# Kernel optimization log

Hardware: AMD Instinct MI355X
Metric: run time of the kernel (lower is better)

Reference implementation:

```python
import jax, jax.numpy as jnp
import numpy as np

V = 50000; C0 = 2000; C1 = 10000   # vocab and adaptive-softmax cutoffs
E = 512; H = 1024; B = 32; T = 128
H1 = H // 4; H2 = H // 16           # div_val = 4.0 per source formula
S1 = C1 - C0; S2 = V - C1


def setup_inputs() -> dict:
    key = jax.random.key(0)
    ks = jax.random.split(key, 12)
    # lengths sorted descending, max length == T (required by output.view(b*(T-1),-1))
    lengths = jnp.sort(jax.random.randint(ks[0], (B,), T // 2, T + 1))[::-1]
    lengths = lengths.at[0].set(T).astype(jnp.int64)
    x = jax.random.randint(ks[1], (B, T), 1, V)
    x = jnp.where(jnp.arange(T)[None, :] < lengths[:, None], x, 0).astype(jnp.int64)  # PAD=0 beyond length
    emb = (jax.random.normal(ks[2], (V, E), jnp.float32) * 0.02).at[0].set(0.0)  # padding_idx=0
    w_ih = jax.random.normal(ks[3], (3 * H, E), jnp.float32) * 0.02
    w_hh = jax.random.normal(ks[4], (3 * H, H), jnp.float32) * 0.02
    b_ih = jnp.zeros((3 * H,), jnp.float32)
    b_hh = jnp.zeros((3 * H,), jnp.float32)
    head_w = jax.random.normal(ks[5], (C0 + 2, H), jnp.float32) * 0.02   # shortlist + 2 cluster logits
    p1 = jax.random.normal(ks[6], (H1, H), jnp.float32) * 0.02
    t1 = jax.random.normal(ks[7], (S1, H1), jnp.float32) * 0.02
    p2 = jax.random.normal(ks[8], (H2, H), jnp.float32) * 0.02
    t2 = jax.random.normal(ks[9], (S2, H2), jnp.float32) * 0.02
    hidden = jnp.zeros((1, B, H), jnp.float32)
    return dict(x=x, lengths=lengths, hidden=hidden, emb=emb, w_ih=w_ih, w_hh=w_hh,
                b_ih=b_ih, b_hh=b_hh, head_w=head_w, p1=p1, t1=t1, p2=p2, t2=t2)


def gru_masked(inp, h0, w_ih, w_hh, b_ih, b_hh, lengths):
    """Torch GRU on packed sequence of lengths-1: frozen hidden + zero outputs past length."""
    xp = jnp.einsum('bte,ge->btg', inp, w_ih) + b_ih  # [B, T-1, 3H] input projections

    def step(h, args):
        xpt, t = args
        hp = h @ w_hh.T + b_hh
        xr, xz, xn = jnp.split(xpt, 3, axis=-1)
        hr, hz, hn = jnp.split(hp, 3, axis=-1)
        r = jax.nn.sigmoid(xr + hr)
        z = jax.nn.sigmoid(xz + hz)
        n = jnp.tanh(xn + r * hn)
        h_new = (1.0 - z) * n + z * h
        valid = (t < lengths - 1)[:, None]
        h = jnp.where(valid, h_new, h)          # freeze hidden past sequence end
        y = jnp.where(valid, h, 0.0)            # pad_packed_sequence zero-fills
        return h, y

    steps = jnp.arange(inp.shape[1])
    hT, ys = jax.lax.scan(step, h0, (jnp.swapaxes(xp, 0, 1), steps))
    return jnp.swapaxes(ys, 0, 1), hT  # [B, T-1, H], [B, H]


def adaptive_loss(out, targets, head_w, p1, t1, p2, t2):
    """AdaptiveLogSoftmaxWithLoss: mean NLL over shortlist + 2 tail clusters."""
    N = out.shape[0]
    head_lp = jax.nn.log_softmax(out @ head_w.T, axis=-1)  # [N, C0+2]
    idx = jnp.arange(N)
    lp_short = head_lp[idx, jnp.clip(targets, 0, C0 - 1)]

    def cluster_lp(p, t, ci, lo, size):
        tail_lp = jax.nn.log_softmax((out @ p.T) @ t.T, axis=-1)  # [N, size]
        rel = jnp.clip(targets - lo, 0, size - 1)
        return head_lp[:, C0 + ci] + tail_lp[idx, rel]

    lp1 = cluster_lp(p1, t1, 0, C0, S1)
    lp2 = cluster_lp(p2, t2, 1, C1, S2)
    logp = jnp.where(targets < C0, lp_short, jnp.where(targets < C1, lp1, lp2))
    return -jnp.mean(logp)


def reference(x, lengths, hidden, emb, w_ih, w_hh, b_ih, b_hh, head_w, p1, t1, p2, t2):
    inp = emb[x][:, :T - 1]  # dropout=0.0 -> identity
    ys, hT = gru_masked(inp, hidden[0], w_ih, w_hh, b_ih, b_hh, lengths)
    out = ys.reshape(B * (T - 1), H)
    targets = x[:, 1:].reshape(-1)
    loss = adaptive_loss(out, targets, head_w, p1, t1, p2, t2)
    return loss, hT[None]
```

## Files before the change

kernel.cpp:

```cpp
#include <hip/hip_runtime.h>
#include <math.h>

#define VV   50000
#define CC0  2000
#define CC1  10000
#define ED   512
#define HD   1024
#define BBATCH 32
#define TT   128
#define HH1  256
#define HH2  64
#define SS1  8000
#define SS2  40000
#define NR   4064
#define G3   3072

#define OFF_XP   0ull
#define OFF_YSB  12484608ull
#define OFF_HB   14565376ull
#define OFF_HT   14598144ull
#define OFF_P1B  14630912ull
#define OFF_P2B  15151104ull
#define OFF_WHB  15281152ull
#define OFF_T1B  16306176ull
#define OFF_PP1  17330176ull
#define OFF_PP2  17461248ull
#define OFF_SUM  17494016ull
#define OFF_LOSS (OFF_SUM + 6ull*4064ull)
#define OFF_INT  (OFF_LOSS + 64ull)

#define ZERO_N (6*4064 + 64)
#define NBG 64

typedef __attribute__((ext_vector_type(8))) __bf16 bf16x8;
typedef __attribute__((ext_vector_type(4))) float f32x4;
typedef __attribute__((ext_vector_type(4))) unsigned int u32x4;
typedef unsigned long long u64;
typedef unsigned short u16;
struct ull2s { u64 x, y; };

__device__ __forceinline__ u16 f2bf(float f) {
    unsigned u = __builtin_bit_cast(unsigned, f);
    u += 0x7fff + ((u >> 16) & 1);
    return (u16)(u >> 16);
}

__global__ void init_k(const float* __restrict__ hidden, u16* __restrict__ hb0,
                       float* __restrict__ zreg, int* __restrict__ cnt1,
                       int* __restrict__ cnt2, int* __restrict__ bar)
{
    int i = blockIdx.x * 256 + threadIdx.x;
    if (i < BBATCH * HD) hb0[i] = f2bf(hidden[i]);
    int zi = i - BBATCH * HD;
    if (zi >= 0 && zi < ZERO_N) zreg[zi] = 0.f;
    if (zi == ZERO_N) { *cnt1 = 0; *cnt2 = 0; }
    int bi = zi - (ZERO_N + 1);
    if (bi >= 0 && bi < 2048) bar[bi] = 0;
}

__global__ void prep_k(const int* __restrict__ x, int* __restrict__ targets,
                       int* __restrict__ hselc, int* __restrict__ list1,
                       int* __restrict__ list2, int* __restrict__ cnt1, int* __restrict__ cnt2)
{
    int n = blockIdx.x * 256 + threadIdx.x;
    if (n >= NR) return;
    int b = n / 127, t = n % 127;
    int tgt = x[b * TT + t + 1];
    targets[n] = tgt;
    hselc[n] = (tgt < CC0) ? tgt : ((tgt < CC1) ? CC0 : CC0 + 1);
    if (tgt >= CC0 && tgt < CC1) list1[atomicAdd(cnt1, 1)] = n;
    else if (tgt >= CC1)         list2[atomicAdd(cnt2, 1)] = n;
}

__global__ void cvt_bf16_k(const float* __restrict__ src, u16* __restrict__ dst, int n4)
{
    int i = blockIdx.x * 256 + threadIdx.x;
    if (i >= n4) return;
    float4 f = *(const float4*)(src + 4 * (size_t)i);
    union { u16 h[4]; u64 v; } u;
    u.h[0] = f2bf(f.x); u.h[1] = f2bf(f.y); u.h[2] = f2bf(f.z); u.h[3] = f2bf(f.w);
    *(u64*)&dst[4 * (size_t)i] = u.v;
}

__global__ void __launch_bounds__(256)
gemm_xp_k(const int* __restrict__ x, const float* __restrict__ emb,
          const float* __restrict__ w_ih, const float* __restrict__ b_ih,
          float* __restrict__ xp)
{
    __shared__ float smem[2 * 16 * 132];
    __shared__ int tok[128];
    float* As = smem;
    float* Ws = smem + 16 * 132;
    const int tid = threadIdx.x;
    const int rbase = blockIdx.x * 128;
    const int cbase = blockIdx.y * 128;
    const int rg = tid >> 4, cg = tid & 15;
    const int rl = tid >> 1;
    const int kk0 = (tid & 1) * 8;

    if (tid < 128) {
        int r = rbase + tid;
        tok[tid] = (r < NR) ? x[(r & 31) * TT + (r >> 5)] : -1;
    }
    __syncthreads();

    float acc[8][8];
#pragma unroll
    for (int i = 0; i < 8; i++)
#pragma unroll
        for (int j = 0; j < 8; j++) acc[i][j] = 0.f;

    for (int k0 = 0; k0 < ED; k0 += 16) {
        int tk = tok[rl];
        float4 a0 = make_float4(0,0,0,0), a1 = a0;
        if (tk >= 0) {
            const float* ap = emb + (size_t)tk * ED + k0 + kk0;
            a0 = *(const float4*)(ap);
            a1 = *(const float4*)(ap + 4);
        }
        As[(kk0+0)*132 + rl] = a0.x; As[(kk0+1)*132 + rl] = a0.y;
        As[(kk0+2)*132 + rl] = a0.z; As[(kk0+3)*132 + rl] = a0.w;
        As[(kk0+4)*132 + rl] = a1.x; As[(kk0+5)*132 + rl] = a1.y;
        As[(kk0+6)*132 + rl] = a1.z; As[(kk0+7)*132 + rl] = a1.w;

        const float* wp = w_ih + (size_t)(cbase + rl) * ED + k0 + kk0;
        float4 w0 = *(const float4*)(wp);
        float4 w1 = *(const float4*)(wp + 4);
        Ws[(kk0+0)*132 + rl] = w0.x; Ws[(kk0+1)*132 + rl] = w0.y;
        Ws[(kk0+2)*132 + rl] = w0.z; Ws[(kk0+3)*132 + rl] = w0.w;
        Ws[(kk0+4)*132 + rl] = w1.x; Ws[(kk0+5)*132 + rl] = w1.y;
        Ws[(kk0+6)*132 + rl] = w1.z; Ws[(kk0+7)*132 + rl] = w1.w;
        __syncthreads();
#pragma unroll
        for (int kk = 0; kk < 16; kk++) {
            float4 va0 = *(float4*)&As[kk*132 + rg*8];
            float4 va1 = *(float4*)&As[kk*132 + rg*8 + 4];
            float4 vw0 = *(float4*)&Ws[kk*132 + cg*8];
            float4 vw1 = *(float4*)&Ws[kk*132 + cg*8 + 4];
            float av[8] = {va0.x,va0.y,va0.z,va0.w,va1.x,va1.y,va1.z,va1.w};
            float wv[8] = {vw0.x,vw0.y,vw0.z,vw0.w,vw1.x,vw1.y,vw1.z,vw1.w};
#pragma unroll
            for (int i = 0; i < 8; i++)
#pragma unroll
                for (int j = 0; j < 8; j++) acc[i][j] += av[i] * wv[j];
        }
        __syncthreads();
    }
#pragma unroll
    for (int i = 0; i < 8; i++) {
        int r = rbase + rg*8 + i;
        if (r >= NR) continue;
#pragma unroll
        for (int j = 0; j < 8; j++) {
            int c = cbase + cg*8 + j;
            xp[(size_t)r * G3 + c] = acc[i][j] + b_ih[c];
        }
    }
}

template<int EPI, int BFP32>
__global__ void __launch_bounds__(256)
mfma_gemm_k(const u16* __restrict__ Ab, const void* __restrict__ Bsrc,
            int Mdirect, int N, int K,
            const int* __restrict__ rowmap, const int* __restrict__ cntp,
            u16* __restrict__ outB, int ldo,
            float* __restrict__ gsum, float* __restrict__ gsel,
            const int* __restrict__ selcol, const int* __restrict__ targets, int lo)
{
    const int M = cntp ? *cntp : Mdirect;
    const int rbase = blockIdx.x * 128;
    if (rbase >= M) return;
    const int cbase = blockIdx.y * 128;

    __shared__ u16 As[128 * 40];
    __shared__ u16 Bs[128 * 40];
    __shared__ const u16* aptr[128];
    __shared__ int rown[128];
    __shared__ float redl[128 * 2];

    const int tid = threadIdx.x;
    if (tid < 128) {
        int rid = -1;
        if (rbase + tid < M) rid = rowmap ? rowmap[rbase + tid] : (rbase + tid);
        rown[tid] = rid;
        aptr[tid] = (rid >= 0) ? (Ab + (size_t)rid * K) : nullptr;
    }
    __syncthreads();

    const int lane = tid & 63, wid = tid >> 6;
    const int n16 = lane & 15, quad = lane >> 4;
    const int m0 = (wid >> 1) * 64, n0 = (wid & 1) * 64;
    const int i = tid >> 1, half = tid & 1;

    f32x4 acc[4][4];
#pragma unroll
    for (int a = 0; a < 4; a++)
#pragma unroll
        for (int b = 0; b < 4; b++) acc[a][b] = (f32x4){0.f, 0.f, 0.f, 0.f};

    for (int k0 = 0; k0 < K; k0 += 32) {
        const u16* ap = aptr[i];
        u32x4 a0 = {0,0,0,0}, a1 = a0;
        if (ap) {
            a0 = *(const u32x4*)(ap + k0 + half * 16);
            a1 = *(const u32x4*)(ap + k0 + half * 16 + 8);
        }
        u32x4 b0 = {0,0,0,0}, b1 = b0;
        int c = cbase + i;
        if (c < N) {
            if (BFP32) {
                const float* bp = (const float*)Bsrc + (size_t)c * K + k0 + half * 16;
                float4 f0 = *(const float4*)(bp);
                float4 f1 = *(const float4*)(bp + 4);
                float4 f2 = *(const float4*)(bp + 8);
                float4 f3 = *(const float4*)(bp + 12);
                union { u16 h[16]; u32x4 v[2]; } u;
                u.h[0]=f2bf(f0.x); u.h[1]=f2bf(f0.y); u.h[2]=f2bf(f0.z); u.h[3]=f2bf(f0.w);
                u.h[4]=f2bf(f1.x); u.h[5]=f2bf(f1.y); u.h[6]=f2bf(f1.z); u.h[7]=f2bf(f1.w);
                u.h[8]=f2bf(f2.x); u.h[9]=f2bf(f2.y); u.h[10]=f2bf(f2.z); u.h[11]=f2bf(f2.w);
                u.h[12]=f2bf(f3.x); u.h[13]=f2bf(f3.y); u.h[14]=f2bf(f3.z); u.h[15]=f2bf(f3.w);
                b0 = u.v[0]; b1 = u.v[1];
            } else {
                const u16* bp = (const u16*)Bsrc + (size_t)c * K + k0 + half * 16;
                b0 = *(const u32x4*)(bp);
                b1 = *(const u32x4*)(bp + 8);
            }
        }
        __syncthreads();
        *(u32x4*)&As[i * 40 + half * 16]     = a0;
        *(u32x4*)&As[i * 40 + half * 16 + 8] = a1;
        *(u32x4*)&Bs[i * 40 + half * 16]     = b0;
        *(u32x4*)&Bs[i * 40 + half * 16 + 8] = b1;
        __syncthreads();

        bf16x8 av[4], bv[4];
#pragma unroll
        for (int mi = 0; mi < 4; mi++)
            av[mi] = *(const bf16x8*)&As[(m0 + mi * 16 + n16) * 40 + quad * 8];
#pragma unroll
        for (int ni = 0; ni < 4; ni++)
            bv[ni] = *(const bf16x8*)&Bs[(n0 + ni * 16 + n16) * 40 + quad * 8];
#pragma unroll
        for (int mi = 0; mi < 4; mi++)
#pragma unroll
            for (int ni = 0; ni < 4; ni++)
                acc[mi][ni] = __builtin_amdgcn_mfma_f32_16x16x32_bf16(
                    av[mi], bv[ni], acc[mi][ni], 0, 0, 0);
    }

    __syncthreads();
    if (EPI == 0) {
#pragma unroll
        for (int mi = 0; mi < 4; mi++)
#pragma unroll
            for (int ni = 0; ni < 4; ni++)
#pragma unroll
                for (int r = 0; r < 4; r++) {
                    int row = rbase + m0 + mi * 16 + quad * 4 + r;
                    int col = cbase + n0 + ni * 16 + n16;
                    if (row < M && col < N)
                        outB[(size_t)row * ldo + col] = f2bf(acc[mi][ni][r]);
                }
    } else {
#pragma unroll
        for (int mi = 0; mi < 4; mi++)
#pragma unroll
            for (int r = 0; r < 4; r++) {
                int lrow = m0 + mi * 16 + quad * 4 + r;
                int nid = rown[lrow];
                float s = 0.f;
                if (nid >= 0) {
                    int sc = (EPI == 1) ? selcol[nid] : (targets[nid] - lo);
#pragma unroll
                    for (int ni = 0; ni < 4; ni++) {
                        int col = cbase + n0 + ni * 16 + n16;
                        if (col < N) {
                            float v = acc[mi][ni][r];
                            s += __expf(v);
                            if (col == sc) gsel[nid] = v;
                        }
                    }
                }
                s += __shfl_xor(s, 1);
                s += __shfl_xor(s, 2);
                s += __shfl_xor(s, 4);
                s += __shfl_xor(s, 8);
                if (n16 == 0) redl[lrow * 2 + (wid & 1)] = s;
            }
        __syncthreads();
        if (tid < 128) {
            int nid = rown[tid];
            if (nid >= 0) atomicAdd(&gsum[nid], redl[tid * 2] + redl[tid * 2 + 1]);
        }
    }
}

__global__ void __launch_bounds__(128, 1)
gru_persist_k(const float* __restrict__ xp, const float* __restrict__ hidden,
              u16* __restrict__ hb0, u16* __restrict__ hb1,
              const float* __restrict__ w_hh, const float* __restrict__ b_hh,
              const int* __restrict__ lengths, u16* __restrict__ ys,
              float* __restrict__ hT, int* __restrict__ arr)
{
    __shared__ u16 Blds[48 * 1032];
    const int tid = threadIdx.x;
    const int bid = blockIdx.x;
    const int j0 = bid * 16;
    const int lane = tid & 63, wid = tid >> 6;
    const int n16 = lane & 15, quad = lane >> 4;

    for (int idx = tid; idx < 48 * 1024; idx += 128) {
        int r = idx >> 10, k = idx & 1023;
        int g = r >> 4, c = r & 15;
        Blds[r * 1032 + k] = f2bf(w_hh[(size_t)(g * HD + j0 + c) * HD + k]);
    }

    const int col = j0 + n16;
    float bh0 = b_hh[col], bh1 = b_hh[HD + col], bh2 = b_hh[2 * HD + col];
    float hold[4];
    int len[4];
#pragma unroll
    for (int r = 0; r < 4; r++) {
        int b = wid * 16 + quad * 4 + r;
        len[r] = lengths[b];
        hold[r] = hidden[b * HD + col];
    }
    __syncthreads();

    for (int t = 0; t < TT - 1; t++) {
        const u16* hb = (t & 1) ? hb1 : hb0;
        u16* hbn = (t & 1) ? hb0 : hb1;

        float xrv[4], xzv[4], xnv[4];
#pragma unroll
        for (int r = 0; r < 4; r++) {
            int b = wid * 16 + quad * 4 + r;
            const float* xpt = xp + ((size_t)t * BBATCH + b) * G3 + col;
            xrv[r] = xpt[0]; xzv[r] = xpt[HD]; xnv[r] = xpt[2 * HD];
        }

        const u16* arow = hb + (size_t)(wid * 16 + n16) * HD + quad * 8;
        u64 apf[64];
#pragma unroll
        for (int ks = 0; ks < 32; ks++) {
            apf[2*ks]   = __hip_atomic_load((const u64*)(arow + ks*32),
                                            __ATOMIC_RELAXED, __HIP_MEMORY_SCOPE_AGENT);
            apf[2*ks+1] = __hip_atomic_load((const u64*)(arow + ks*32 + 4),
                                            __ATOMIC_RELAXED, __HIP_MEMORY_SCOPE_AGENT);
        }

        f32x4 acc0 = {0.f, 0.f, 0.f, 0.f}, acc1 = acc0, acc2 = acc0;
        const int boff = n16 * 1032 + quad * 8;
#pragma unroll
        for (int ks = 0; ks < 32; ks++) {
            ull2s av2; av2.x = apf[2*ks]; av2.y = apf[2*ks+1];
            bf16x8 av = __builtin_bit_cast(bf16x8, av2);
            bf16x8 b0 = *(const bf16x8*)&Blds[boff + ks*32];
            bf16x8 b1 = *(const bf16x8*)&Blds[16*1032 + boff + ks*32];
            bf16x8 b2 = *(const bf16x8*)&Blds[32*1032 + boff + ks*32];
            acc0 = __builtin_amdgcn_mfma_f32_16x16x32_bf16(av, b0, acc0, 0, 0, 0);
            acc1 = __builtin_amdgcn_mfma_f32_16x16x32_bf16(av, b1, acc1, 0, 0, 0);
            acc2 = __builtin_amdgcn_mfma_f32_16x16x32_bf16(av, b2, acc2, 0, 0, 0);
        }

#pragma unroll
        for (int r = 0; r < 4; r++) {
            int b = wid * 16 + quad * 4 + r;
            float hr = acc0[r] + bh0, hz = acc1[r] + bh1, hn = acc2[r] + bh2;
            float rg = 1.f / (1.f + __expf(-(xrv[r] + hr)));
            float zg = 1.f / (1.f + __expf(-(xzv[r] + hz)));
            float nv = tanhf(xnv[r] + rg * hn);
            bool valid = t < (len[r] - 1);
            float hnew = valid ? (1.f - zg) * nv + zg * hold[r] : hold[r];
            hold[r] = hnew;
            __hip_atomic_store(hbn + (size_t)b * HD + col, f2bf(hnew),
                               __ATOMIC_RELAXED, __HIP_MEMORY_SCOPE_AGENT);
            ys[((size_t)b * 127 + t) * HD + col] = f2bf(valid ? hnew : 0.f);
            if (t == TT - 2) hT[b * HD + col] = hnew;
        }

        __syncthreads();
        if (tid < 64) {
            if (tid == 0) {
                __builtin_amdgcn_s_waitcnt(0);
                __hip_atomic_store(&arr[bid * 32], t + 1, __ATOMIC_RELAXED,
                                   __HIP_MEMORY_SCOPE_AGENT);
            }
            int guard = 0;
            while (__hip_atomic_load(&arr[tid * 32], __ATOMIC_RELAXED,
                                     __HIP_MEMORY_SCOPE_AGENT) < t + 1
                   && guard < (1 << 20)) {
                __builtin_amdgcn_s_sleep(1);
                guard++;
            }
        }
        asm volatile("" ::: "memory");
        __syncthreads();
    }
}

__global__ void finish_k(const float* __restrict__ hsum, const float* __restrict__ hsel,
                         const float* __restrict__ t1sum, const float* __restrict__ t1sel,
                         const float* __restrict__ t2sum, const float* __restrict__ t2sel,
                         const int* __restrict__ targets, float* __restrict__ losssum)
{
    __shared__ float red[256];
    int n = blockIdx.x * 256 + threadIdx.x;
    float lp = 0.f;
    if (n < NR) {
        lp = hsel[n] - logf(hsum[n]);
        int tgt = targets[n];
        if (tgt >= CC1)      lp += t2sel[n] - logf(t2sum[n]);
        else if (tgt >= CC0) lp += t1sel[n] - logf(t1sum[n]);
    }
    red[threadIdx.x] = lp;
    __syncthreads();
    for (int s = 128; s > 0; s >>= 1) {
        if (threadIdx.x < s) red[threadIdx.x] += red[threadIdx.x + s];
        __syncthreads();
    }
    if (threadIdx.x == 0) atomicAdd(losssum, red[0]);
}

__global__ void out_k(const float* __restrict__ losssum, const float* __restrict__ hT,
                      float* __restrict__ out)
{
    int i = blockIdx.x * 256 + threadIdx.x;
    if (i == 0) out[0] = -losssum[0] / (float)NR;
    if (i < BBATCH * HD) out[1 + i] = hT[i];
}

extern "C" void kernel_launch(void* const* d_in, const int* in_sizes, int n_in,
                              void* d_out, int out_size, void* d_ws, size_t ws_size,
                              hipStream_t stream)
{
    const int*   x       = (const int*)d_in[0];
    const int*   lengths = (const int*)d_in[1];
    const float* hidden  = (const float*)d_in[2];
    const float* emb     = (const float*)d_in[3];
    const float* w_ih    = (const float*)d_in[4];
    const float* w_hh    = (const float*)d_in[5];
    const float* b_ih    = (const float*)d_in[6];
    const float* b_hh    = (const float*)d_in[7];
    const float* head_w  = (const float*)d_in[8];
    const float* p1      = (const float*)d_in[9];
    const float* t1      = (const float*)d_in[10];
    const float* p2      = (const float*)d_in[11];
    const float* t2      = (const float*)d_in[12];

    float* ws = (float*)d_ws;
    float* xp    = ws + OFF_XP;
    u16*   ysb   = (u16*)(ws + OFF_YSB);
    u16*   hb0   = (u16*)(ws + OFF_HB);
    u16*   hb1   = hb0 + BBATCH * HD;
    float* hT    = ws + OFF_HT;
    u16*   p1b   = (u16*)(ws + OFF_P1B);
    u16*   p2b   = (u16*)(ws + OFF_P2B);
    u16*   whb   = (u16*)(ws + OFF_WHB);
    u16*   t1b   = (u16*)(ws + OFF_T1B);
    u16*   pp1b  = (u16*)(ws + OFF_PP1);
    u16*   pp2b  = (u16*)(ws + OFF_PP2);
    float* hsum  = ws + OFF_SUM;
    float* hsel  = hsum + 4064;
    float* t1sum = hsel + 4064;
    float* t1sel = t1sum + 4064;
    float* t2sum = t1sel + 4064;
    float* t2sel = t2sum + 4064;
    float* losss = ws + OFF_LOSS;
    int* ib      = (int*)(ws + OFF_INT);
    int* targets = ib;
    int* hselc   = ib + 4064;
    int* list1   = ib + 2 * 4064;
    int* list2   = ib + 3 * 4064;
    int* cnt1    = ib + 4 * 4064;
    int* cnt2    = cnt1 + 1;
    int* bar     = ib + 5 * 4064;

    float* out = (float*)d_out;

    init_k<<<232, 256, 0, stream>>>(hidden, hb0, hsum, cnt1, cnt2, bar);
    prep_k<<<16, 256, 0, stream>>>(x, targets, hselc, list1, list2, cnt1, cnt2);

    cvt_bf16_k<<<(512512 + 255) / 256, 256, 0, stream>>>(head_w, whb, 512512);
    cvt_bf16_k<<<(512000 + 255) / 256, 256, 0, stream>>>(t1, t1b, 512000);
    cvt_bf16_k<<<(65536 + 255) / 256, 256, 0, stream>>>(p1, pp1b, 65536);
    cvt_bf16_k<<<(16384 + 255) / 256, 256, 0, stream>>>(p2, pp2b, 16384);

    gemm_xp_k<<<dim3(32, 24), 256, 0, stream>>>(x, emb, w_ih, b_ih, xp);

    gru_persist_k<<<NBG, 128, 0, stream>>>(xp, hidden, hb0, hb1, w_hh, b_hh,
                                           lengths, ysb, hT, bar);

    mfma_gemm_k<0, 0><<<dim3(32, 2), 256, 0, stream>>>(
        ysb, pp1b, NR, HH1, HD, nullptr, nullptr, p1b, HH1,
        nullptr, nullptr, nullptr, nullptr, 0);
    mfma_gemm_k<0, 0><<<dim3(32, 1), 256, 0, stream>>>(
        ysb, pp2b, NR, HH2, HD, nullptr, nullptr, p2b, HH2,
        nullptr, nullptr, nullptr, nullptr, 0);
    mfma_gemm_k<1, 0><<<dim3(32, 16), 256, 0, stream>>>(
        ysb, whb, NR, CC0 + 2, HD, nullptr, nullptr, nullptr, 0,
        hsum, hsel, hselc, nullptr, 0);
    mfma_gemm_k<2, 0><<<dim3(32, 63), 256, 0, stream>>>(
        p1b, t1b, 0, SS1, HH1, list1, cnt1, nullptr, 0,
        t1sum, t1sel, nullptr, targets, CC0);
    mfma_gemm_k<2, 1><<<dim3(32, 313), 256, 0, stream>>>(
        p2b, t2, 0, SS2, HH2, list2, cnt2, nullptr, 0,
        t2sum, t2sel, nullptr, targets, CC1);

    finish_k<<<16, 256, 0, stream>>>(hsum, hsel, t1sum, t1sel, t2sum, t2sel,
                                     targets, losss);
    out_k<<<128, 256, 0, stream>>>(losss, hT, out);
}
```

Baseline: 1.540 ms.

## Move input projection GEMM to bf16 MFMA and pre-convert t2 to bf16

Replaces the fp32 FMA embedding×w_ih GEMM with a bf16 gather kernel, a w_ih conversion, and the existing MFMA GEMM using a new epilogue that adds the bias and writes fp32 xp. It also converts t2 to bf16 once into the xp buffer after the GRU has consumed it, so the tail-2 GEMM uses the bf16 B path. The aim is to cut the cost of the pre-GRU projection with matrix cores, in exchange for bf16 rounding of the GRU inputs and several workspace buffers being reused (embA in the ysb slot, w_ih in the head_w slot before head_w is converted).

New measurement: 1.427 ms. -7.4%, faster.

```diff
diff --git a/kernel.cpp b/kernel.cpp
--- a/kernel.cpp
+++ b/kernel.cpp
@@ -82,80 +82,22 @@
     *(u64*)&dst[4 * (size_t)i] = u.v;
 }
 
-__global__ void __launch_bounds__(256)
-gemm_xp_k(const int* __restrict__ x, const float* __restrict__ emb,
-          const float* __restrict__ w_ih, const float* __restrict__ b_ih,
-          float* __restrict__ xp)
-{
-    __shared__ float smem[2 * 16 * 132];
-    __shared__ int tok[128];
-    float* As = smem;
-    float* Ws = smem + 16 * 132;
-    const int tid = threadIdx.x;
-    const int rbase = blockIdx.x * 128;
-    const int cbase = blockIdx.y * 128;
-    const int rg = tid >> 4, cg = tid & 15;
-    const int rl = tid >> 1;
-    const int kk0 = (tid & 1) * 8;
-
-    if (tid < 128) {
-        int r = rbase + tid;
-        tok[tid] = (r < NR) ? x[(r & 31) * TT + (r >> 5)] : -1;
-    }
-    __syncthreads();
-
-    float acc[8][8];
-#pragma unroll
-    for (int i = 0; i < 8; i++)
-#pragma unroll
-        for (int j = 0; j < 8; j++) acc[i][j] = 0.f;
-
-    for (int k0 = 0; k0 < ED; k0 += 16) {
-        int tk = tok[rl];
-        float4 a0 = make_float4(0,0,0,0), a1 = a0;
-        if (tk >= 0) {
-            const float* ap = emb + (size_t)tk * ED + k0 + kk0;
-            a0 = *(const float4*)(ap);
-            a1 = *(const float4*)(ap + 4);
-        }
-        As[(kk0+0)*132 + rl] = a0.x; As[(kk0+1)*132 + rl] = a0.y;
-        As[(kk0+2)*132 + rl] = a0.z; As[(kk0+3)*132 + rl] = a0.w;
-        As[(kk0+4)*132 + rl] = a1.x; As[(kk0+5)*132 + rl] = a1.y;
-        As[(kk0+6)*132 + rl] = a1.z; As[(kk0+7)*132 + rl] = a1.w;
-
-        const float* wp = w_ih + (size_t)(cbase + rl) * ED + k0 + kk0;
-        float4 w0 = *(const float4*)(wp);
-        float4 w1 = *(const float4*)(wp + 4);
-        Ws[(kk0+0)*132 + rl] = w0.x; Ws[(kk0+1)*132 + rl] = w0.y;
-        Ws[(kk0+2)*132 + rl] = w0.z; Ws[(kk0+3)*132 + rl] = w0.w;
-        Ws[(kk0+4)*132 + rl] = w1.x; Ws[(kk0+5)*132 + rl] = w1.y;
-        Ws[(kk0+6)*132 + rl] = w1.z; Ws[(kk0+7)*132 + rl] = w1.w;
-        __syncthreads();
-#pragma unroll
-        for (int kk = 0; kk < 16; kk++) {
-            float4 va0 = *(float4*)&As[kk*132 + rg*8];
-            float4 va1 = *(float4*)&As[kk*132 + rg*8 + 4];
-            float4 vw0 = *(float4*)&Ws[kk*132 + cg*8];
-            float4 vw1 = *(float4*)&Ws[kk*132 + cg*8 + 4];
-            float av[8] = {va0.x,va0.y,va0.z,va0.w,va1.x,va1.y,va1.z,va1.w};
-            float wv[8] = {vw0.x,vw0.y,vw0.z,vw0.w,vw1.x,vw1.y,vw1.z,vw1.w};
-#pragma unroll
-            for (int i = 0; i < 8; i++)
-#pragma unroll
-                for (int j = 0; j < 8; j++) acc[i][j] += av[i] * wv[j];
-        }
-        __syncthreads();
-    }
-#pragma unroll
-    for (int i = 0; i < 8; i++) {
-        int r = rbase + rg*8 + i;
-        if (r >= NR) continue;
-#pragma unroll
-        for (int j = 0; j < 8; j++) {
-            int c = cbase + cg*8 + j;
-            xp[(size_t)r * G3 + c] = acc[i][j] + b_ih[c];
-        }
-    }
+__global__ void emb_gather_k(const int* __restrict__ x, const float* __restrict__ emb,
+                             u16* __restrict__ embA)
+{
+    int idx = blockIdx.x * 256 + threadIdx.x;
+    if (idx >= NR * 64) return;
+    int n = idx >> 6;
+    int kk = (idx & 63) << 3;
+    int b = n & 31, t = n >> 5;
+    int tok = x[b * TT + t];
+    const float* ap = emb + (size_t)tok * ED + kk;
+    float4 f0 = *(const float4*)ap;
+    float4 f1 = *(const float4*)(ap + 4);
+    union { u16 h[8]; u32x4 v; } u;
+    u.h[0] = f2bf(f0.x); u.h[1] = f2bf(f0.y); u.h[2] = f2bf(f0.z); u.h[3] = f2bf(f0.w);
+    u.h[4] = f2bf(f1.x); u.h[5] = f2bf(f1.y); u.h[6] = f2bf(f1.z); u.h[7] = f2bf(f1.w);
+    *(u32x4*)&embA[(size_t)n * ED + kk] = u.v;
 }
 
 template<int EPI, int BFP32>
@@ -260,6 +202,18 @@
                     int col = cbase + n0 + ni * 16 + n16;
                     if (row < M && col < N)
                         outB[(size_t)row * ldo + col] = f2bf(acc[mi][ni][r]);
+                }
+    } else if (EPI == 3) {
+#pragma unroll
+        for (int mi = 0; mi < 4; mi++)
+#pragma unroll
+            for (int ni = 0; ni < 4; ni++)
+#pragma unroll
+                for (int r = 0; r < 4; r++) {
+                    int row = rbase + m0 + mi * 16 + quad * 4 + r;
+                    int col = cbase + n0 + ni * 16 + n16;
+                    if (row < M && col < N)
+                        gsum[(size_t)row * ldo + col] = acc[mi][ni][r] + gsel[col];
                 }
     } else {
 #pragma unroll
@@ -476,20 +430,30 @@
     int* cnt2    = cnt1 + 1;
     int* bar     = ib + 5 * 4064;
 
+    u16* embA = (u16*)(ws + OFF_YSB);
+    u16* wihb = (u16*)(ws + OFF_WHB);
+    u16* t2b  = (u16*)(ws + OFF_XP);
+
     float* out = (float*)d_out;
 
     init_k<<<232, 256, 0, stream>>>(hidden, hb0, hsum, cnt1, cnt2, bar);
     prep_k<<<16, 256, 0, stream>>>(x, targets, hselc, list1, list2, cnt1, cnt2);
+
+    emb_gather_k<<<(NR * 64 + 255) / 256, 256, 0, stream>>>(x, emb, embA);
+    cvt_bf16_k<<<(393216 + 255) / 256, 256, 0, stream>>>(w_ih, wihb, 393216);
+    mfma_gemm_k<3, 0><<<dim3(32, 24), 256, 0, stream>>>(
+        embA, wihb, NR, G3, ED, nullptr, nullptr, nullptr, G3,
+        xp, (float*)b_ih, nullptr, nullptr, 0);
 
     cvt_bf16_k<<<(512512 + 255) / 256, 256, 0, stream>>>(head_w, whb, 512512);
     cvt_bf16_k<<<(512000 + 255) / 256, 256, 0, stream>>>(t1, t1b, 512000);
     cvt_bf16_k<<<(65536 + 255) / 256, 256, 0, stream>>>(p1, pp1b, 65536);
     cvt_bf16_k<<<(16384 + 255) / 256, 256, 0, stream>>>(p2, pp2b, 16384);
 
-    gemm_xp_k<<<dim3(32, 24), 256, 0, stream>>>(x, emb, w_ih, b_ih, xp);
-
     gru_persist_k<<<NBG, 128, 0, stream>>>(xp, hidden, hb0, hb1, w_hh, b_hh,
                                            lengths, ysb, hT, bar);
+
+    cvt_bf16_k<<<(640000 + 255) / 256, 256, 0, stream>>>(t2, t2b, 640000);
 
     mfma_gemm_k<0, 0><<<dim3(32, 2), 256, 0, stream>>>(
         ysb, pp1b, NR, HH1, HD, nullptr, nullptr, p1b, HH1,
@@ -503,8 +467,8 @@
     mfma_gemm_k<2, 0><<<dim3(32, 63), 256, 0, stream>>>(
         p1b, t1b, 0, SS1, HH1, list1, cnt1, nullptr, 0,
         t1sum, t1sel, nullptr, targets, CC0);
-    mfma_gemm_k<2, 1><<<dim3(32, 313), 256, 0, stream>>>(
-        p2b, t2, 0, SS2, HH2, list2, cnt2, nullptr, 0,
+    mfma_gemm_k<2, 0><<<dim3(32, 313), 256, 0, stream>>>(
+        p2b, t2b, 0, SS2, HH2, list2, cnt2, nullptr, 0,
         t2sum, t2sel, nullptr, targets, CC1);
 
     finish_k<<<16, 256, 0, stream>>>(hsum, hsel, t1sum, t1sel, t2sum, t2sel,
```
